# Optimization experiments

Hardware: AMD Instinct MI355X
Metric: run time of the kernel (lower is better)

The kernel has to match this reference:

```python
import jax, jax.numpy as jnp
import numpy as np

N_NODES = 100000
N_EDGES = 1600000
DIM_IN, DIM_U, DIM_OUT = 48, 128, 128
N_PASS = 2


def setup_inputs() -> dict:
    key = jax.random.key(0)
    ks = jax.random.split(key, 9)
    y = jax.random.normal(ks[0], (N_NODES, DIM_IN), dtype=jnp.float32)
    start_nodes = jax.random.randint(ks[1], (N_EDGES,), 0, N_NODES)
    end_nodes = jax.random.randint(ks[2], (N_EDGES,), 0, N_NODES)
    degree_factors_start = jax.random.uniform(ks[3], (N_EDGES, 1), dtype=jnp.float32)
    degree_factors = jax.random.uniform(ks[4], (N_NODES, 1), dtype=jnp.float32)
    # MLP params (n_U_layers=2 -> one hidden Linear(dim_in->dim_U) + output Linear(dim_U->dim_out))
    s1 = 1.0 / np.sqrt(DIM_IN)
    s2 = 1.0 / np.sqrt(DIM_U)
    W1 = jax.random.uniform(ks[5], (DIM_IN, DIM_U), minval=-s1, maxval=s1, dtype=jnp.float32)
    b1 = jax.random.uniform(ks[6], (DIM_U,), minval=-s1, maxval=s1, dtype=jnp.float32)
    W2 = jax.random.uniform(ks[7], (DIM_U, DIM_OUT), minval=-s2, maxval=s2, dtype=jnp.float32)
    b2 = jax.random.uniform(ks[8], (DIM_OUT,), minval=-s2, maxval=s2, dtype=jnp.float32)
    return {"y": y, "start_nodes": start_nodes, "end_nodes": end_nodes,
            "degree_factors_start": degree_factors_start, "degree_factors": degree_factors,
            "W1": W1, "b1": b1, "W2": W2, "b2": b2}


def reference(y, start_nodes, end_nodes, degree_factors_start, degree_factors, W1, b1, W2, b2):
    n_nodes = degree_factors.shape[0]
    for _ in range(N_PASS):
        # gather source features, scale by start-degree factor -> [n_edges, d]
        msg = y[start_nodes] * degree_factors_start
        # scatter_sum over destination nodes, scale by end-degree factor -> [n_nodes, d]
        y = jax.ops.segment_sum(msg, end_nodes, num_segments=n_nodes) * degree_factors
    # update MLP: hidden layer with relu, then output projection
    h = jax.nn.relu(y @ W1 + b1)
    out = h @ W2 + b2
    return (out, start_nodes, end_nodes, degree_factors_start, degree_factors)
```

## Files before the change

### kernel.cpp

```cpp
#include <hip/hip_runtime.h>
#include <stddef.h>

#define N_NODES 100000
#define N_EDGES 1600000
#define DIM_IN  48
#define DIM_U   128
#define DIM_OUT 128


typedef float nf4 __attribute__((ext_vector_type(4)));

#define B_BKT     196
#define BKT_SHIFT 9
#define NPB       512
#define AP_WGS    256
#define EDGES_PER_WG ((N_EDGES + AP_WGS - 1) / AP_WGS)
#define BKT_CAP   10240

__global__ __launch_bounds__(256) void histcount_kernel(const int* __restrict__ en,
                                                        int* __restrict__ partial) {
    __shared__ int lh[B_BKT];
    int w = blockIdx.x, t = threadIdx.x;
    for (int i = t; i < B_BKT; i += 256) lh[i] = 0;
    __syncthreads();
    int lo = w * EDGES_PER_WG;
    int hi = min(lo + EDGES_PER_WG, N_EDGES);
    for (int i = lo + t; i < hi; i += 256)
        atomicAdd(&lh[((unsigned)en[i]) >> BKT_SHIFT], 1);
    __syncthreads();
    for (int b = t; b < B_BKT; b += 256)
        partial[b * AP_WGS + w] = lh[b];
}

__global__ __launch_bounds__(256) void colscan_kernel(int* __restrict__ partial,
                                                      int* __restrict__ bcnt) {
    __shared__ int part[256];
    int b = blockIdx.x, t = threadIdx.x;
    int v = partial[b * AP_WGS + t];
    part[t] = v;
    __syncthreads();
    for (int off = 1; off < 256; off <<= 1) {
        int u = (t >= off) ? part[t - off] : 0;
        __syncthreads();
        part[t] += u;
        __syncthreads();
    }
    partial[b * AP_WGS + t] = part[t] - v;
    if (t == 255) bcnt[b] = part[255];
}

__global__ __launch_bounds__(256) void bscan_kernel(const int* __restrict__ bcnt,
                                                    int* __restrict__ bbase) {
    __shared__ int part[256];
    int t = threadIdx.x;
    int v = (t < B_BKT) ? bcnt[t] : 0;
    part[t] = v;
    __syncthreads();
    for (int off = 1; off < 256; off <<= 1) {
        int u = (t >= off) ? part[t - off] : 0;
        __syncthreads();
        part[t] += u;
        __syncthreads();
    }
    if (t < B_BKT) bbase[t] = part[t] - v;
    if (t == 0) bbase[B_BKT] = N_EDGES;
}

__global__ __launch_bounds__(256) void scatter_rb_kernel(const int* __restrict__ sn,
                                                         const int* __restrict__ en,
                                                         const float* __restrict__ dfs,
                                                         const int* __restrict__ partial,
                                                         const int* __restrict__ bbase,
                                                         int2* __restrict__ rb) {
    __shared__ int lh[B_BKT];
    __shared__ int basec[B_BKT];
    int w = blockIdx.x, t = threadIdx.x;
    for (int i = t; i < B_BKT; i += 256) {
        lh[i] = 0;
        basec[i] = bbase[i] + partial[i * AP_WGS + w];
    }
    __syncthreads();
    int lo = w * EDGES_PER_WG;
    int hi = min(lo + EDGES_PER_WG, N_EDGES);
    for (int i = lo + t; i < hi; i += 256) {
        int e = en[i];
        int b = ((unsigned)e) >> BKT_SHIFT;
        int r = atomicAdd(&lh[b], 1);
        int pos = basec[b] + r;
        unsigned packed = (unsigned)sn[i] | (((unsigned)e & (NPB - 1)) << 17);
        rb[pos] = make_int2((int)packed, __float_as_int(dfs[i]));
    }
}

__global__ __launch_bounds__(512) void bucket_fill_kernel(const int2* __restrict__ rb,
                                                          const int* __restrict__ bbase,
                                                          int* __restrict__ rowptr,
                                                          int2* __restrict__ pe,
                                                          int n_nodes) {
    __shared__ int2 stage[BKT_CAP];
    __shared__ int ldeg[NPB];
    __shared__ int lscan[NPB];
    int b = blockIdx.x, t = threadIdx.x;
    int lo = bbase[b], hi = bbase[b + 1];
    int cnt = hi - lo;
    for (int i = t; i < NPB; i += 512) ldeg[i] = 0;
    __syncthreads();
    for (int i = t; i < cnt; i += 512) {
        int2 r = rb[lo + i];
        if (i < BKT_CAP) stage[i] = r;
        atomicAdd(&ldeg[((unsigned)r.x) >> 17], 1);
    }
    __syncthreads();
    int v = ldeg[t];
    lscan[t] = v;
    __syncthreads();
    for (int off = 1; off < 512; off <<= 1) {
        int u = (t >= off) ? lscan[t - off] : 0;
        __syncthreads();
        lscan[t] += u;
        __syncthreads();
    }
    int excl = lscan[t] - v;
    int node = b * NPB + t;
    if (node < n_nodes) rowptr[node] = lo + excl;
    if (b == B_BKT - 1 && t == 0) rowptr[n_nodes] = N_EDGES;
    ldeg[t] = lo + excl;
    __syncthreads();
    for (int i = t; i < cnt; i += 512) {
        int2 r = (i < BKT_CAP) ? stage[i] : rb[lo + i];
        int dl = ((unsigned)r.x) >> 17;
        int pos = atomicAdd(&ldeg[dl], 1);
        pe[pos] = make_int2(r.x & 0x1FFFF, r.y);
    }
}

__global__ __launch_bounds__(192) void prop_kernel(const float* __restrict__ yin,
                                                   float* __restrict__ yout,
                                                   const int* __restrict__ rowptr,
                                                   const int2* __restrict__ pe,
                                                   const float* __restrict__ dfn,
                                                   int n_nodes) {
    int n = blockIdx.x * 16 + threadIdx.y;
    if (n >= n_nodes) return;
    int d4 = threadIdx.x * 4;
    int lo = rowptr[n];
    int hi = rowptr[n + 1];
    float4 acc = make_float4(0.f, 0.f, 0.f, 0.f);
    int e = lo;
    for (; e + 8 <= hi; e += 8) {
        int2 e0 = pe[e],     e1 = pe[e + 1], e2 = pe[e + 2], e3 = pe[e + 3];
        int2 e4 = pe[e + 4], e5 = pe[e + 5], e6 = pe[e + 6], e7 = pe[e + 7];
        float4 v0 = *(const float4*)&yin[(size_t)e0.x * DIM_IN + d4];
        float4 v1 = *(const float4*)&yin[(size_t)e1.x * DIM_IN + d4];
        float4 v2 = *(const float4*)&yin[(size_t)e2.x * DIM_IN + d4];
        float4 v3 = *(const float4*)&yin[(size_t)e3.x * DIM_IN + d4];
        float4 v4 = *(const float4*)&yin[(size_t)e4.x * DIM_IN + d4];
        float4 v5 = *(const float4*)&yin[(size_t)e5.x * DIM_IN + d4];
        float4 v6 = *(const float4*)&yin[(size_t)e6.x * DIM_IN + d4];
        float4 v7 = *(const float4*)&yin[(size_t)e7.x * DIM_IN + d4];
        float w0 = __int_as_float(e0.y), w1 = __int_as_float(e1.y);
        float w2 = __int_as_float(e2.y), w3 = __int_as_float(e3.y);
        float w4 = __int_as_float(e4.y), w5 = __int_as_float(e5.y);
        float w6 = __int_as_float(e6.y), w7 = __int_as_float(e7.y);
        acc.x = fmaf(v0.x, w0, acc.x); acc.y = fmaf(v0.y, w0, acc.y);
        acc.z = fmaf(v0.z, w0, acc.z); acc.w = fmaf(v0.w, w0, acc.w);
        acc.x = fmaf(v1.x, w1, acc.x); acc.y = fmaf(v1.y, w1, acc.y);
        acc.z = fmaf(v1.z, w1, acc.z); acc.w = fmaf(v1.w, w1, acc.w);
        acc.x = fmaf(v2.x, w2, acc.x); acc.y = fmaf(v2.y, w2, acc.y);
        acc.z = fmaf(v2.z, w2, acc.z); acc.w = fmaf(v2.w, w2, acc.w);
        acc.x = fmaf(v3.x, w3, acc.x); acc.y = fmaf(v3.y, w3, acc.y);
        acc.z = fmaf(v3.z, w3, acc.z); acc.w = fmaf(v3.w, w3, acc.w);
        acc.x = fmaf(v4.x, w4, acc.x); acc.y = fmaf(v4.y, w4, acc.y);
        acc.z = fmaf(v4.z, w4, acc.z); acc.w = fmaf(v4.w, w4, acc.w);
        acc.x = fmaf(v5.x, w5, acc.x); acc.y = fmaf(v5.y, w5, acc.y);
        acc.z = fmaf(v5.z, w5, acc.z); acc.w = fmaf(v5.w, w5, acc.w);
        acc.x = fmaf(v6.x, w6, acc.x); acc.y = fmaf(v6.y, w6, acc.y);
        acc.z = fmaf(v6.z, w6, acc.z); acc.w = fmaf(v6.w, w6, acc.w);
        acc.x = fmaf(v7.x, w7, acc.x); acc.y = fmaf(v7.y, w7, acc.y);
        acc.z = fmaf(v7.z, w7, acc.z); acc.w = fmaf(v7.w, w7, acc.w);
    }
    for (; e + 4 <= hi; e += 4) {
        int2 e0 = pe[e], e1 = pe[e + 1], e2 = pe[e + 2], e3 = pe[e + 3];
        float4 v0 = *(const float4*)&yin[(size_t)e0.x * DIM_IN + d4];
        float4 v1 = *(const float4*)&yin[(size_t)e1.x * DIM_IN + d4];
        float4 v2 = *(const float4*)&yin[(size_t)e2.x * DIM_IN + d4];
        float4 v3 = *(const float4*)&yin[(size_t)e3.x * DIM_IN + d4];
        float w0 = __int_as_float(e0.y), w1 = __int_as_float(e1.y);
        float w2 = __int_as_float(e2.y), w3 = __int_as_float(e3.y);
        acc.x = fmaf(v0.x, w0, acc.x); acc.y = fmaf(v0.y, w0, acc.y);
        acc.z = fmaf(v0.z, w0, acc.z); acc.w = fmaf(v0.w, w0, acc.w);
        acc.x = fmaf(v1.x, w1, acc.x); acc.y = fmaf(v1.y, w1, acc.y);
        acc.z = fmaf(v1.z, w1, acc.z); acc.w = fmaf(v1.w, w1, acc.w);
        acc.x = fmaf(v2.x, w2, acc.x); acc.y = fmaf(v2.y, w2, acc.y);
        acc.z = fmaf(v2.z, w2, acc.z); acc.w = fmaf(v2.w, w2, acc.w);
        acc.x = fmaf(v3.x, w3, acc.x); acc.y = fmaf(v3.y, w3, acc.y);
        acc.z = fmaf(v3.z, w3, acc.z); acc.w = fmaf(v3.w, w3, acc.w);
    }
    for (; e < hi; ++e) {
        int2 ee = pe[e];
        float w = __int_as_float(ee.y);
        float4 v = *(const float4*)&yin[(size_t)ee.x * DIM_IN + d4];
        acc.x = fmaf(v.x, w, acc.x); acc.y = fmaf(v.y, w, acc.y);
        acc.z = fmaf(v.z, w, acc.z); acc.w = fmaf(v.w, w, acc.w);
    }
    if (dfn) {
        float s = dfn[n];
        acc.x *= s; acc.y *= s; acc.z *= s; acc.w *= s;
    }
    *(float4*)&yout[(size_t)n * DIM_IN + d4] = acc;
}

__global__ __launch_bounds__(192) void scatter1_kernel(
    const float* __restrict__ yin, float* __restrict__ yout,
    const int* __restrict__ sn, const int* __restrict__ en,
    const float* __restrict__ dfs, int E)
{
    int e = blockIdx.x * 4 + threadIdx.y;
    if (e >= E) return;
    int d = threadIdx.x;
    int s = sn[e], dn = en[e];
    float v = yin[(size_t)s * DIM_IN + d] * dfs[e];
    atomicAdd(&yout[(size_t)dn * DIM_IN + d], v);
}
__global__ __launch_bounds__(192) void scatter2_kernel(
    const float* __restrict__ yin, float* __restrict__ yout,
    const int* __restrict__ sn, const int* __restrict__ en,
    const float* __restrict__ dfs, const float* __restrict__ df, int E)
{
    int e = blockIdx.x * 4 + threadIdx.y;
    if (e >= E) return;
    int d = threadIdx.x;
    int s = sn[e], dn = en[e];
    float w = dfs[e] * df[s];
    float v = yin[(size_t)s * DIM_IN + d] * w;
    atomicAdd(&yout[(size_t)dn * DIM_IN + d], v);
}
__global__ __launch_bounds__(256) void zerof_kernel(float* __restrict__ p, int n) {
    int i = blockIdx.x * 256 + threadIdx.x;
    if (i < n) p[i] = 0.0f;
}

__global__ __launch_bounds__(256) void mlp_kernel(const float* __restrict__ y2,
                                                  const float* __restrict__ df,
                                                  const float* __restrict__ W1,
                                                  const float* __restrict__ b1,
                                                  const float* __restrict__ W2,
                                                  const float* __restrict__ b2,
                                                  float* __restrict__ out,
                                                  int n_nodes) {
    __shared__ float xs[64 * DIM_IN];
    __shared__ float hs[64 * DIM_U];
    int node0 = blockIdx.x * 64;
    int t = threadIdx.x;

    for (int i4 = t; i4 < 64 * DIM_IN / 4; i4 += 256) {
        int n = node0 + i4 / (DIM_IN / 4);
        float4 v = make_float4(0.f, 0.f, 0.f, 0.f);
        if (n < n_nodes) {
            v = *(const float4*)&y2[(size_t)node0 * DIM_IN + (size_t)i4 * 4];
            float s = df[n];
            v.x *= s; v.y *= s; v.z *= s; v.w *= s;
        }
        *(float4*)&xs[i4 * 4] = v;
    }
    __syncthreads();

    int cg = t & 31;
    int ng = t >> 5;

    float acc[8][4];
    #pragma unroll
    for (int m = 0; m < 8; ++m)
        #pragma unroll
        for (int c = 0; c < 4; ++c) acc[m][c] = 0.f;
    const float* xbase = &xs[ng * 8 * DIM_IN];
    for (int k = 0; k < DIM_IN; ++k) {
        float4 wv = *(const float4*)&W1[k * DIM_U + cg * 4];
        #pragma unroll
        for (int m = 0; m < 8; ++m) {
            float xv = xbase[m * DIM_IN + k];
            acc[m][0] = fmaf(xv, wv.x, acc[m][0]);
            acc[m][1] = fmaf(xv, wv.y, acc[m][1]);
            acc[m][2] = fmaf(xv, wv.z, acc[m][2]);
            acc[m][3] = fmaf(xv, wv.w, acc[m][3]);
        }
    }
    {
        float4 bb = *(const float4*)&b1[cg * 4];
        #pragma unroll
        for (int m = 0; m < 8; ++m) {
            float4 h;
            h.x = fmaxf(acc[m][0] + bb.x, 0.f);
            h.y = fmaxf(acc[m][1] + bb.y, 0.f);
            h.z = fmaxf(acc[m][2] + bb.z, 0.f);
            h.w = fmaxf(acc[m][3] + bb.w, 0.f);
            *(float4*)&hs[(ng * 8 + m) * DIM_U + cg * 4] = h;
        }
    }
    __syncthreads();

    float acc2[8][4];
    #pragma unroll
    for (int m = 0; m < 8; ++m)
        #pragma unroll
        for (int c = 0; c < 4; ++c) acc2[m][c] = 0.f;
    const float* hbase = &hs[ng * 8 * DIM_U];
    for (int k = 0; k < DIM_U; ++k) {
        float4 wv = *(const float4*)&W2[k * DIM_OUT + cg * 4];
        #pragma unroll
        for (int m = 0; m < 8; ++m) {
            float hv = hbase[m * DIM_U + k];
            acc2[m][0] = fmaf(hv, wv.x, acc2[m][0]);
            acc2[m][1] = fmaf(hv, wv.y, acc2[m][1]);
            acc2[m][2] = fmaf(hv, wv.z, acc2[m][2]);
            acc2[m][3] = fmaf(hv, wv.w, acc2[m][3]);
        }
    }
    {
        float4 bb = *(const float4*)&b2[cg * 4];
        #pragma unroll
        for (int m = 0; m < 8; ++m) {
            int n = node0 + ng * 8 + m;
            if (n < n_nodes) {
                float4 o;
                o.x = acc2[m][0] + bb.x;
                o.y = acc2[m][1] + bb.y;
                o.z = acc2[m][2] + bb.z;
                o.w = acc2[m][3] + bb.w;
                *(float4*)&out[(size_t)n * DIM_OUT + cg * 4] = o;
            }
        }
    }
}

__global__ __launch_bounds__(256) void tail_kernel(
    const int* __restrict__ sn, const int* __restrict__ en,
    const float* __restrict__ dfs, const float* __restrict__ df,
    float* __restrict__ out)
{
    int i = blockIdx.x * 256 + threadIdx.x;
    const int E = N_EDGES, N = N_NODES;
    int total = 3 * E + N;
    if (i >= total) return;
    float v;
    if (i < E) v = (float)sn[i];
    else if (i < 2 * E) v = (float)en[i - E];
    else if (i < 3 * E) v = dfs[i - 2 * E];
    else v = df[i - 3 * E];
    __builtin_nontemporal_store(v, &out[(size_t)N * DIM_OUT + (size_t)i]);
}

extern "C" void kernel_launch(void* const* d_in, const int* in_sizes, int n_in,
                              void* d_out, int out_size, void* d_ws, size_t ws_size,
                              hipStream_t stream) {
    const float* y   = (const float*)d_in[0];
    const int* start = (const int*)d_in[1];
    const int* endn  = (const int*)d_in[2];
    const float* dfs = (const float*)d_in[3];
    const float* df  = (const float*)d_in[4];
    const float* W1  = (const float*)d_in[5];
    const float* b1  = (const float*)d_in[6];
    const float* W2  = (const float*)d_in[7];
    const float* b2  = (const float*)d_in[8];
    float* out = (float*)d_out;

    const int N = N_NODES, E = N_EDGES;
    const size_t Y_ELEMS = (size_t)N * DIM_IN;

    char* ws = (char*)d_ws;
    size_t off = 0;
    auto carve = [&](size_t bytes) -> void* {
        void* p = ws + off;
        off = (off + bytes + 255) & ~(size_t)255;
        return p;
    };
    int*   rowptr  = (int*)carve((size_t)(N + 1) * 4);
    int*   partial = (int*)carve((size_t)B_BKT * AP_WGS * 4);
    int*   bcnt    = (int*)carve((size_t)B_BKT * 4);
    int*   bbase   = (int*)carve((size_t)(B_BKT + 1) * 4);
    int2*  pedge   = (int2*)carve((size_t)E * 8);
    float* y1      = (float*)carve(Y_ELEMS * 4);
    float* y2      = (float*)carve(Y_ELEMS * 4);
    size_t CSR_NEED = off;

    if (ws_size >= CSR_NEED) {
        histcount_kernel<<<AP_WGS, 256, 0, stream>>>(endn, partial);
        colscan_kernel<<<B_BKT, 256, 0, stream>>>(partial, bcnt);
        bscan_kernel<<<1, 256, 0, stream>>>(bcnt, bbase);
        scatter_rb_kernel<<<AP_WGS, 256, 0, stream>>>(start, endn, dfs, partial,
                                                      bbase, pedge);
        bucket_fill_kernel<<<B_BKT, 512, 0, stream>>>(pedge, bbase, rowptr,
                                                      pedge, N);
        prop_kernel<<<(N + 15) / 16, dim3(12, 16), 0, stream>>>(y, y1, rowptr, pedge,
                                                                df, N);
        prop_kernel<<<(N + 15) / 16, dim3(12, 16), 0, stream>>>(y1, y2, rowptr, pedge,
                                                                nullptr, N);
    } else {
        float* fy1 = (float*)d_ws;
        float* fy2 = fy1 + Y_ELEMS;
        y2 = fy2;
        int zn = (int)(2 * Y_ELEMS);
        zerof_kernel<<<(zn + 255) / 256, 256, 0, stream>>>(fy1, zn);
        scatter1_kernel<<<(E + 3) / 4, dim3(48, 4), 0, stream>>>(y, fy1, start, endn,
                                                                 dfs, E);
        scatter2_kernel<<<(E + 3) / 4, dim3(48, 4), 0, stream>>>(fy1, fy2, start, endn,
                                                                 dfs, df, E);
    }

    mlp_kernel<<<(N + 63) / 64, 256, 0, stream>>>(y2, df, W1, b1, W2, b2, out, N);

    {
        int total = 3 * E + N;
        tail_kernel<<<(total + 255) / 256, 256, 0, stream>>>(start, endn, dfs, df, out);
    }
}
```

Measured before the change: 328.1 us.

## Sort nodes by in-degree for load-balanced propagation and double CSR build workgroups

Adds a counting sort of nodes by in-degree (histogram, column scan, bin scan, scatter) that produces a permutation. The propagation kernels then process nodes in that order, so the 16 nodes sharing a workgroup have similar edge counts and fewer lanes sit idle. Separately, the CSR build now uses twice as many histogram and scatter workgroups. The cost is four extra small kernel launches and one extra indirection per node, and neighbouring rows in the grid no longer write neighbouring output rows.

Measured after the change: 343.9 us. 4.8% more time.

```diff
diff --git a/kernel.cpp b/kernel.cpp
--- a/kernel.cpp
+++ b/kernel.cpp
@@ -13,9 +13,12 @@
 #define B_BKT     196
 #define BKT_SHIFT 9
 #define NPB       512
-#define AP_WGS    256
+#define AP_WGS    512
 #define EDGES_PER_WG ((N_EDGES + AP_WGS - 1) / AP_WGS)
 #define BKT_CAP   10240
+
+#define DEG_WGS   391
+#define DBINS     64
 
 __global__ __launch_bounds__(256) void histcount_kernel(const int* __restrict__ en,
                                                         int* __restrict__ partial) {
@@ -32,21 +35,21 @@
         partial[b * AP_WGS + w] = lh[b];
 }
 
-__global__ __launch_bounds__(256) void colscan_kernel(int* __restrict__ partial,
-                                                      int* __restrict__ bcnt) {
-    __shared__ int part[256];
+__global__ __launch_bounds__(AP_WGS) void colscan_kernel(int* __restrict__ partial,
+                                                         int* __restrict__ bcnt) {
+    __shared__ int part[AP_WGS];
     int b = blockIdx.x, t = threadIdx.x;
     int v = partial[b * AP_WGS + t];
     part[t] = v;
     __syncthreads();
-    for (int off = 1; off < 256; off <<= 1) {
+    for (int off = 1; off < AP_WGS; off <<= 1) {
         int u = (t >= off) ? part[t - off] : 0;
         __syncthreads();
         part[t] += u;
         __syncthreads();
     }
     partial[b * AP_WGS + t] = part[t] - v;
-    if (t == 255) bcnt[b] = part[255];
+    if (t == AP_WGS - 1) bcnt[b] = part[AP_WGS - 1];
 }
 
 __global__ __launch_bounds__(256) void bscan_kernel(const int* __restrict__ bcnt,
@@ -134,14 +137,84 @@
     }
 }
 
+__global__ __launch_bounds__(256) void deghist_kernel(const int* __restrict__ rowptr,
+                                                      int* __restrict__ dpart,
+                                                      int n_nodes) {
+    __shared__ int lh[DBINS];
+    int w = blockIdx.x, t = threadIdx.x;
+    if (t < DBINS) lh[t] = 0;
+    __syncthreads();
+    int n = w * 256 + t;
+    if (n < n_nodes) {
+        int deg = rowptr[n + 1] - rowptr[n];
+        atomicAdd(&lh[min(deg, DBINS - 1)], 1);
+    }
+    __syncthreads();
+    if (t < DBINS) dpart[t * DEG_WGS + w] = lh[t];
+}
+__global__ __launch_bounds__(512) void degcolscan_kernel(int* __restrict__ dpart,
+                                                         int* __restrict__ dcnt) {
+    __shared__ int part[512];
+    int b = blockIdx.x, t = threadIdx.x;
+    int v = (t < DEG_WGS) ? dpart[b * DEG_WGS + t] : 0;
+    part[t] = v;
+    __syncthreads();
+    for (int off = 1; off < 512; off <<= 1) {
+        int u = (t >= off) ? part[t - off] : 0;
+        __syncthreads();
+        part[t] += u;
+        __syncthreads();
+    }
+    if (t < DEG_WGS) dpart[b * DEG_WGS + t] = part[t] - v;
+    if (t == 511) dcnt[b] = part[511];
+}
+__global__ __launch_bounds__(64) void degbinscan_kernel(const int* __restrict__ dcnt,
+                                                        int* __restrict__ dbase) {
+    __shared__ int part[DBINS];
+    int t = threadIdx.x;
+    int v = dcnt[t];
+    part[t] = v;
+    __syncthreads();
+    for (int off = 1; off < DBINS; off <<= 1) {
+        int u = (t >= off) ? part[t - off] : 0;
+        __syncthreads();
+        part[t] += u;
+        __syncthreads();
+    }
+    dbase[t] = part[t] - v;
+}
+__global__ __launch_bounds__(256) void degscatter_kernel(const int* __restrict__ rowptr,
+                                                         const int* __restrict__ dpart,
+                                                         const int* __restrict__ dbase,
+                                                         int* __restrict__ perm,
+                                                         int n_nodes) {
+    __shared__ int lh[DBINS];
+    __shared__ int basec[DBINS];
+    int w = blockIdx.x, t = threadIdx.x;
+    if (t < DBINS) {
+        lh[t] = 0;
+        basec[t] = dbase[t] + dpart[t * DEG_WGS + w];
+    }
+    __syncthreads();
+    int n = w * 256 + t;
+    if (n < n_nodes) {
+        int deg = rowptr[n + 1] - rowptr[n];
+        int bin = min(deg, DBINS - 1);
+        int r = atomicAdd(&lh[bin], 1);
+        perm[basec[bin] + r] = n;
+    }
+}
+
 __global__ __launch_bounds__(192) void prop_kernel(const float* __restrict__ yin,
                                                    float* __restrict__ yout,
                                                    const int* __restrict__ rowptr,
                                                    const int2* __restrict__ pe,
+                                                   const int* __restrict__ perm,
                                                    const float* __restrict__ dfn,
                                                    int n_nodes) {
-    int n = blockIdx.x * 16 + threadIdx.y;
-    if (n >= n_nodes) return;
+    int ni = blockIdx.x * 16 + threadIdx.y;
+    if (ni >= n_nodes) return;
+    int n = perm[ni];
     int d4 = threadIdx.x * 4;
     int lo = rowptr[n];
     int hi = rowptr[n + 1];
@@ -378,6 +451,10 @@
     int*   partial = (int*)carve((size_t)B_BKT * AP_WGS * 4);
     int*   bcnt    = (int*)carve((size_t)B_BKT * 4);
     int*   bbase   = (int*)carve((size_t)(B_BKT + 1) * 4);
+    int*   dpart   = (int*)carve((size_t)DBINS * DEG_WGS * 4);
+    int*   dcnt    = (int*)carve((size_t)DBINS * 4);
+    int*   dbase   = (int*)carve((size_t)DBINS * 4);
+    int*   perm    = (int*)carve((size_t)N * 4);
     int2*  pedge   = (int2*)carve((size_t)E * 8);
     float* y1      = (float*)carve(Y_ELEMS * 4);
     float* y2      = (float*)carve(Y_ELEMS * 4);
@@ -385,16 +462,20 @@
 
     if (ws_size >= CSR_NEED) {
         histcount_kernel<<<AP_WGS, 256, 0, stream>>>(endn, partial);
-        colscan_kernel<<<B_BKT, 256, 0, stream>>>(partial, bcnt);
+        colscan_kernel<<<B_BKT, AP_WGS, 0, stream>>>(partial, bcnt);
         bscan_kernel<<<1, 256, 0, stream>>>(bcnt, bbase);
         scatter_rb_kernel<<<AP_WGS, 256, 0, stream>>>(start, endn, dfs, partial,
                                                       bbase, pedge);
         bucket_fill_kernel<<<B_BKT, 512, 0, stream>>>(pedge, bbase, rowptr,
                                                       pedge, N);
+        deghist_kernel<<<DEG_WGS, 256, 0, stream>>>(rowptr, dpart, N);
+        degcolscan_kernel<<<DBINS, 512, 0, stream>>>(dpart, dcnt);
+        degbinscan_kernel<<<1, DBINS, 0, stream>>>(dcnt, dbase);
+        degscatter_kernel<<<DEG_WGS, 256, 0, stream>>>(rowptr, dpart, dbase, perm, N);
         prop_kernel<<<(N + 15) / 16, dim3(12, 16), 0, stream>>>(y, y1, rowptr, pedge,
-                                                                df, N);
+                                                                perm, df, N);
         prop_kernel<<<(N + 15) / 16, dim3(12, 16), 0, stream>>>(y1, y2, rowptr, pedge,
-                                                                nullptr, N);
+                                                                perm, nullptr, N);
     } else {
         float* fy1 = (float*)d_ws;
         float* fy2 = fy1 + Y_ELEMS;
```

## Fold bucket scan into consumers and merge tail copy into MLP kernel

Applied to the files above, without the earlier changes.

Removes the single-block bucket-offset scan kernel: scatter_rb and bucket_fill now each recompute the prefix scan of bucket counts in shared memory. The output-copy tail kernel is merged into the MLP launch as extra grid-stride blocks, so its memory traffic can overlap with MLP compute. This cuts two launches and inter-kernel gaps, at the cost of redundant per-block scans and an extra 512-wide scan with more barriers in bucket_fill.

New measurement: 325.3 us (median of 2 runs). Within noise of the previous version (-0.8%).

```diff
diff --git a/kernel.cpp b/kernel.cpp
--- a/kernel.cpp
+++ b/kernel.cpp
@@ -17,6 +17,9 @@
 #define EDGES_PER_WG ((N_EDGES + AP_WGS - 1) / AP_WGS)
 #define BKT_CAP   10240
 
+#define MLPB      ((N_NODES + 63) / 64)
+#define TAILB     4096
+
 __global__ __launch_bounds__(256) void histcount_kernel(const int* __restrict__ en,
                                                         int* __restrict__ partial) {
     __shared__ int lh[B_BKT];
@@ -49,35 +52,28 @@
     if (t == 255) bcnt[b] = part[255];
 }
 
-__global__ __launch_bounds__(256) void bscan_kernel(const int* __restrict__ bcnt,
-                                                    int* __restrict__ bbase) {
-    __shared__ int part[256];
-    int t = threadIdx.x;
-    int v = (t < B_BKT) ? bcnt[t] : 0;
-    part[t] = v;
-    __syncthreads();
-    for (int off = 1; off < 256; off <<= 1) {
-        int u = (t >= off) ? part[t - off] : 0;
-        __syncthreads();
-        part[t] += u;
-        __syncthreads();
-    }
-    if (t < B_BKT) bbase[t] = part[t] - v;
-    if (t == 0) bbase[B_BKT] = N_EDGES;
-}
-
 __global__ __launch_bounds__(256) void scatter_rb_kernel(const int* __restrict__ sn,
                                                          const int* __restrict__ en,
                                                          const float* __restrict__ dfs,
                                                          const int* __restrict__ partial,
-                                                         const int* __restrict__ bbase,
+                                                         const int* __restrict__ bcnt,
                                                          int2* __restrict__ rb) {
     __shared__ int lh[B_BKT];
     __shared__ int basec[B_BKT];
+    __shared__ int sc[256];
     int w = blockIdx.x, t = threadIdx.x;
-    for (int i = t; i < B_BKT; i += 256) {
-        lh[i] = 0;
-        basec[i] = bbase[i] + partial[i * AP_WGS + w];
+    int v = (t < B_BKT) ? bcnt[t] : 0;
+    sc[t] = v;
+    __syncthreads();
+    for (int off = 1; off < 256; off <<= 1) {
+        int u = (t >= off) ? sc[t - off] : 0;
+        __syncthreads();
+        sc[t] += u;
+        __syncthreads();
+    }
+    if (t < B_BKT) {
+        lh[t] = 0;
+        basec[t] = (sc[t] - v) + partial[t * AP_WGS + w];
     }
     __syncthreads();
     int lo = w * EDGES_PER_WG;
@@ -93,15 +89,28 @@
 }
 
 __global__ __launch_bounds__(512) void bucket_fill_kernel(const int2* __restrict__ rb,
-                                                          const int* __restrict__ bbase,
+                                                          const int* __restrict__ bcnt,
                                                           int* __restrict__ rowptr,
                                                           int2* __restrict__ pe,
                                                           int n_nodes) {
     __shared__ int2 stage[BKT_CAP];
     __shared__ int ldeg[NPB];
     __shared__ int lscan[NPB];
+    __shared__ int sc[512];
+    __shared__ int s_lo, s_hi;
     int b = blockIdx.x, t = threadIdx.x;
-    int lo = bbase[b], hi = bbase[b + 1];
+    int v = (t < B_BKT) ? bcnt[t] : 0;
+    sc[t] = v;
+    __syncthreads();
+    for (int off = 1; off < 512; off <<= 1) {
+        int u = (t >= off) ? sc[t - off] : 0;
+        __syncthreads();
+        sc[t] += u;
+        __syncthreads();
+    }
+    if (t == b) { s_lo = sc[t] - v; s_hi = sc[t]; }
+    __syncthreads();
+    int lo = s_lo, hi = s_hi;
     int cnt = hi - lo;
     for (int i = t; i < NPB; i += 512) ldeg[i] = 0;
     __syncthreads();
@@ -111,8 +120,8 @@
         atomicAdd(&ldeg[((unsigned)r.x) >> 17], 1);
     }
     __syncthreads();
-    int v = ldeg[t];
-    lscan[t] = v;
+    int dv = ldeg[t];
+    lscan[t] = dv;
     __syncthreads();
     for (int off = 1; off < 512; off <<= 1) {
         int u = (t >= off) ? lscan[t - off] : 0;
@@ -120,7 +129,7 @@
         lscan[t] += u;
         __syncthreads();
     }
-    int excl = lscan[t] - v;
+    int excl = lscan[t] - dv;
     int node = b * NPB + t;
     if (node < n_nodes) rowptr[node] = lo + excl;
     if (b == B_BKT - 1 && t == 0) rowptr[n_nodes] = N_EDGES;
@@ -240,18 +249,33 @@
     if (i < n) p[i] = 0.0f;
 }
 
-__global__ __launch_bounds__(256) void mlp_kernel(const float* __restrict__ y2,
-                                                  const float* __restrict__ df,
-                                                  const float* __restrict__ W1,
-                                                  const float* __restrict__ b1,
-                                                  const float* __restrict__ W2,
-                                                  const float* __restrict__ b2,
-                                                  float* __restrict__ out,
-                                                  int n_nodes) {
+__global__ __launch_bounds__(256) void mlp_tail_kernel(
+    const float* __restrict__ y2, const float* __restrict__ df,
+    const float* __restrict__ W1, const float* __restrict__ b1,
+    const float* __restrict__ W2, const float* __restrict__ b2,
+    const int* __restrict__ sn, const int* __restrict__ en,
+    const float* __restrict__ dfs,
+    float* __restrict__ out, int n_nodes)
+{
     __shared__ float xs[64 * DIM_IN];
     __shared__ float hs[64 * DIM_U];
+    int t = threadIdx.x;
+
+    if (blockIdx.x >= MLPB) {
+        const int E = N_EDGES, Nn = N_NODES;
+        int total = 3 * E + Nn;
+        for (int i = (blockIdx.x - MLPB) * 256 + t; i < total; i += TAILB * 256) {
+            float v;
+            if (i < E) v = (float)sn[i];
+            else if (i < 2 * E) v = (float)en[i - E];
+            else if (i < 3 * E) v = dfs[i - 2 * E];
+            else v = df[i - 3 * E];
+            __builtin_nontemporal_store(v, &out[(size_t)Nn * DIM_OUT + (size_t)i]);
+        }
+        return;
+    }
+
     int node0 = blockIdx.x * 64;
-    int t = threadIdx.x;
 
     for (int i4 = t; i4 < 64 * DIM_IN / 4; i4 += 256) {
         int n = node0 + i4 / (DIM_IN / 4);
@@ -331,23 +355,6 @@
             }
         }
     }
-}
-
-__global__ __launch_bounds__(256) void tail_kernel(
-    const int* __restrict__ sn, const int* __restrict__ en,
-    const float* __restrict__ dfs, const float* __restrict__ df,
-    float* __restrict__ out)
-{
-    int i = blockIdx.x * 256 + threadIdx.x;
-    const int E = N_EDGES, N = N_NODES;
-    int total = 3 * E + N;
-    if (i >= total) return;
-    float v;
-    if (i < E) v = (float)sn[i];
-    else if (i < 2 * E) v = (float)en[i - E];
-    else if (i < 3 * E) v = dfs[i - 2 * E];
-    else v = df[i - 3 * E];
-    __builtin_nontemporal_store(v, &out[(size_t)N * DIM_OUT + (size_t)i]);
 }
 
 extern "C" void kernel_launch(void* const* d_in, const int* in_sizes, int n_in,
@@ -377,7 +384,6 @@
     int*   rowptr  = (int*)carve((size_t)(N + 1) * 4);
     int*   partial = (int*)carve((size_t)B_BKT * AP_WGS * 4);
     int*   bcnt    = (int*)carve((size_t)B_BKT * 4);
-    int*   bbase   = (int*)carve((size_t)(B_BKT + 1) * 4);
     int2*  pedge   = (int2*)carve((size_t)E * 8);
     float* y1      = (float*)carve(Y_ELEMS * 4);
     float* y2      = (float*)carve(Y_ELEMS * 4);
@@ -386,10 +392,9 @@
     if (ws_size >= CSR_NEED) {
         histcount_kernel<<<AP_WGS, 256, 0, stream>>>(endn, partial);
         colscan_kernel<<<B_BKT, 256, 0, stream>>>(partial, bcnt);
-        bscan_kernel<<<1, 256, 0, stream>>>(bcnt, bbase);
         scatter_rb_kernel<<<AP_WGS, 256, 0, stream>>>(start, endn, dfs, partial,
-                                                      bbase, pedge);
-        bucket_fill_kernel<<<B_BKT, 512, 0, stream>>>(pedge, bbase, rowptr,
+                                                      bcnt, pedge);
+        bucket_fill_kernel<<<B_BKT, 512, 0, stream>>>(pedge, bcnt, rowptr,
                                                       pedge, N);
         prop_kernel<<<(N + 15) / 16, dim3(12, 16), 0, stream>>>(y, y1, rowptr, pedge,
                                                                 df, N);
@@ -407,10 +412,6 @@
                                                                  dfs, df, E);
     }
 
-    mlp_kernel<<<(N + 63) / 64, 256, 0, stream>>>(y2, df, W1, b1, W2, b2, out, N);
-
-    {
-        int total = 3 * E + N;
-        tail_kernel<<<(total + 255) / 256, 256, 0, stream>>>(start, endn, dfs, df, out);
-    }
-}
+    mlp_tail_kernel<<<MLPB + TAILB, 256, 0, stream>>>(
+        y2, df, W1, b1, W2, b2, start, endn, dfs, out, N);
+}
```
